# Optimization experiments

Hardware: AMD Instinct MI355X
Metric: run time of the kernel (lower is better)

The kernel has to match this reference:

```python
import jax, jax.numpy as jnp
import numpy as np

N = 100000
E = 1600000
IN_CH, HID_CH, OUT_CH = 128, 64, 32


def setup_inputs() -> dict:
    key = jax.random.key(0)
    ks = jax.random.split(key, 6)
    x = jax.random.normal(ks[0], (N, IN_CH), dtype=jnp.float32)
    ei = jax.random.randint(ks[1], (2, E), 0, N, dtype=jnp.int64)
    W1 = jax.random.normal(ks[2], (IN_CH, HID_CH), dtype=jnp.float32) * 0.05
    b1 = jax.random.normal(ks[3], (HID_CH,), dtype=jnp.float32) * 0.05
    W2 = jax.random.normal(ks[4], (HID_CH, OUT_CH), dtype=jnp.float32) * 0.05
    b2 = jax.random.normal(ks[5], (OUT_CH,), dtype=jnp.float32) * 0.05
    return {"x": x, "ei": ei, "W1": W1, "b1": b1, "W2": W2, "b2": b2}


def gcn_layer(x, sa, da, n):
    # degree with self-loops already appended in sa/da
    deg = jax.ops.segment_sum(jnp.ones((sa.shape[0],), x.dtype), da, num_segments=n)
    prod = deg[sa] * deg[da]
    norm = jnp.where(prod > 0, jax.lax.rsqrt(prod), 0.0)  # (deg_s*deg_d)^-0.5, inf->0
    msg = x[sa] * norm[:, None]            # [E+N, C] gather + scale
    return jax.ops.segment_sum(msg, da, num_segments=n)  # scatter_add


def reference(x, ei, W1, b1, W2, b2):
    n = x.shape[0]
    loop = jnp.arange(n, dtype=ei.dtype)
    sa = jnp.concatenate([ei[0], loop])
    da = jnp.concatenate([ei[1], loop])
    h = gcn_layer(x @ W1 + b1, sa, da, n)
    h = jax.nn.relu(h)
    # dropout: eval mode (training=False) -> identity
    return gcn_layer(h @ W2 + b2, sa, da, n)
```

## Files before the change

kernel.cpp:

```cpp
#include <hip/hip_runtime.h>

#define NN 100000
#define NE 1600000
#define IN_CH 128
#define HID_CH 64
#define OUT_CH 32
#define NBUCK 391
#define CHUNKA 8192

typedef unsigned short ushort_t;

__device__ inline ushort_t f2bf(float f) {
    union { float f; unsigned u; } v; v.f = f;
    unsigned r = v.u + 0x7fff + ((v.u >> 16) & 1);
    return (ushort_t)(r >> 16);
}
__device__ inline float blo(unsigned u) {
    union { unsigned x; float f; } v; v.x = u << 16; return v.f;
}
__device__ inline float bhi(unsigned u) {
    union { unsigned x; float f; } v; v.x = u & 0xffff0000u; return v.f;
}

__global__ __launch_bounds__(256) void k_bhist(const int* __restrict__ da,
                                               int* __restrict__ bcnt) {
    __shared__ int hist[NBUCK];
    int t = threadIdx.x;
    for (int i = t; i < NBUCK; i += 256) hist[i] = 0;
    __syncthreads();
    int base = blockIdx.x * CHUNKA;
    for (int i = 0; i < CHUNKA; i += 256) {
        int e = base + i + t;
        if (e < NE) atomicAdd(&hist[da[e] >> 8], 1);
    }
    __syncthreads();
    for (int i = t; i < NBUCK; i += 256) {
        int c = hist[i];
        if (c) atomicAdd(&bcnt[i], c);
    }
}

__global__ __launch_bounds__(512) void k_bscan(const int* __restrict__ bcnt,
                                               int* __restrict__ bbase,
                                               int* __restrict__ bcur,
                                               int* __restrict__ rowptr) {
    __shared__ int lds[512];
    int t = threadIdx.x;
    int v = (t < NBUCK) ? bcnt[t] : 0;
    lds[t] = v;
    __syncthreads();
    for (int off = 1; off < 512; off <<= 1) {
        int x = (t >= off) ? lds[t - off] : 0;
        __syncthreads();
        lds[t] += x;
        __syncthreads();
    }
    int excl = lds[t] - v;
    if (t < NBUCK) { bbase[t] = excl; bcur[t] = excl; }
    if (t == 0) { bbase[NBUCK] = NE; rowptr[NN] = NE; }
}

__global__ __launch_bounds__(256) void k_bfill(const int* __restrict__ sa,
                                               const int* __restrict__ da,
                                               int* __restrict__ bcur,
                                               unsigned* __restrict__ ebuf) {
    __shared__ int hist[NBUCK];
    __shared__ int lcur[NBUCK];
    int t = threadIdx.x;
    for (int i = t; i < NBUCK; i += 256) hist[i] = 0;
    __syncthreads();
    int base = blockIdx.x * CHUNKA;
    for (int i = 0; i < CHUNKA; i += 256) {
        int e = base + i + t;
        if (e < NE) atomicAdd(&hist[da[e] >> 8], 1);
    }
    __syncthreads();
    for (int b = t; b < NBUCK; b += 256) {
        int c = hist[b];
        lcur[b] = c ? atomicAdd(&bcur[b], c) : 0;
    }
    __syncthreads();
    for (int i = 0; i < CHUNKA; i += 256) {
        int e = base + i + t;
        if (e < NE) {
            int d = da[e];
            int p = atomicAdd(&lcur[d >> 8], 1);
            ebuf[p] = ((unsigned)sa[e] << 8) | (unsigned)(d & 255);
        }
    }
}

__global__ __launch_bounds__(256) void k_bfine(const unsigned* __restrict__ ebuf,
                                               const int* __restrict__ bbase,
                                               int* __restrict__ rowptr,
                                               float* __restrict__ rs,
                                               int* __restrict__ col) {
    __shared__ int cnt[256];
    __shared__ int cur[256];
    __shared__ int scn[256];
    int b = blockIdx.x, t = threadIdx.x;
    int nb = NN - b * 256; if (nb > 256) nb = 256;
    int beg = bbase[b], end = bbase[b + 1];
    cnt[t] = 0;
    __syncthreads();
    for (int i = beg + t; i < end; i += 256) atomicAdd(&cnt[ebuf[i] & 255], 1);
    __syncthreads();
    int v = cnt[t];
    scn[t] = v;
    __syncthreads();
    for (int off = 1; off < 256; off <<= 1) {
        int x = (t >= off) ? scn[t - off] : 0;
        __syncthreads();
        scn[t] += x;
        __syncthreads();
    }
    int excl = scn[t] - v;
    if (t < nb) {
        rowptr[b * 256 + t] = beg + excl;
        rs[b * 256 + t] = rsqrtf((float)(v + 1));
        cur[t] = beg + excl;
    }
    __syncthreads();
    for (int i = beg + t; i < end; i += 256) {
        unsigned p = ebuf[i];
        int pos = atomicAdd(&cur[p & 255], 1);
        col[pos] = (int)(p >> 8);
    }
}

#define SWZ1(n, k) ((n) * 128 + ((k) ^ ((((n) & 7)) << 2)))
#define SWZ2(n, k) ((n) * 64 + ((k) ^ ((((n) & 7)) << 2)))

__global__ __launch_bounds__(256) void k_gemm1(
    const float* __restrict__ x, const float* __restrict__ W1,
    const float* __restrict__ b1, const float* __restrict__ rs,
    ushort_t* __restrict__ xsb) {
    __shared__ float xt[64 * 128];
    __shared__ float w1s[128 * 64];
    int t = threadIdx.x;
    int base = blockIdx.x * 64;

#pragma unroll
    for (int i = 0; i < 8; ++i) {
        int flat = i * 1024 + t * 4;
        int node = flat >> 7, k0 = flat & 127;
        int gn = base + node;
        float4 v = make_float4(0.f, 0.f, 0.f, 0.f);
        if (gn < NN) v = *(const float4*)(x + (size_t)gn * IN_CH + k0);
        *(float4*)&xt[SWZ1(node, k0)] = v;
        *(float4*)&w1s[flat] = *(const float4*)(W1 + flat);
    }
    __syncthreads();

    int tn = t & 15, tc = t >> 4;
    int c0 = tc * 4;
    float acc[4][4];
#pragma unroll
    for (int a = 0; a < 4; ++a)
#pragma unroll
        for (int b = 0; b < 4; ++b) acc[a][b] = 0.f;

    for (int k0 = 0; k0 < 128; k0 += 4) {
        float xq[4][4], wq[4][4];
#pragma unroll
        for (int j = 0; j < 4; ++j)
            *(float4*)&wq[j][0] = *(float4*)&w1s[(k0 + j) * 64 + c0];
#pragma unroll
        for (int jn = 0; jn < 4; ++jn)
            *(float4*)&xq[jn][0] = *(float4*)&xt[SWZ1(tn + jn * 16, k0)];
#pragma unroll
        for (int jn = 0; jn < 4; ++jn)
#pragma unroll
            for (int j = 0; j < 4; ++j)
#pragma unroll
                for (int jc = 0; jc < 4; ++jc)
                    acc[jn][jc] = fmaf(xq[jn][j], wq[j][jc], acc[jn][jc]);
    }

    float4 bb = *(const float4*)&b1[c0];
#pragma unroll
    for (int jn = 0; jn < 4; ++jn) {
        int gn = base + tn + jn * 16;
        if (gn < NN) {
            float r = rs[gn];
            uint2 pk;
            pk.x = (unsigned)f2bf((acc[jn][0] + bb.x) * r) |
                   ((unsigned)f2bf((acc[jn][1] + bb.y) * r) << 16);
            pk.y = (unsigned)f2bf((acc[jn][2] + bb.z) * r) |
                   ((unsigned)f2bf((acc[jn][3] + bb.w) * r) << 16);
            *(uint2*)&xsb[(size_t)gn * HID_CH + c0] = pk;
        }
    }
}

__global__ __launch_bounds__(256) void k_agg1(
    const int* __restrict__ rowptr, const int* __restrict__ col,
    const ushort_t* __restrict__ xsb, const float* __restrict__ rs,
    float* __restrict__ h) {
    int gid = blockIdx.x * blockDim.x + threadIdx.x;
    int n = gid >> 6;
    if (n >= NN) return;
    int lane = threadIdx.x & 63;
    int g = lane >> 4;
    unsigned c0 = (unsigned)(lane & 15) * 4;
    int beg = rowptr[n], end = rowptr[n + 1];

    float a0 = 0.f, a1 = 0.f, a2 = 0.f, a3 = 0.f;
    if (g == 0) {
        uint2 sv = *(const uint2*)&xsb[(unsigned)n * 64u + c0];
        a0 = blo(sv.x); a1 = bhi(sv.x); a2 = blo(sv.y); a3 = bhi(sv.y);
    }

    int i = beg;
    for (; i + 8 <= end; i += 8) {
        int s0 = col[i + g];
        int s1 = col[i + 4 + g];
        uint2 v0 = *(const uint2*)&xsb[(unsigned)s0 * 64u + c0];
        uint2 v1 = *(const uint2*)&xsb[(unsigned)s1 * 64u + c0];
        a0 += blo(v0.x); a1 += bhi(v0.x); a2 += blo(v0.y); a3 += bhi(v0.y);
        a0 += blo(v1.x); a1 += bhi(v1.x); a2 += blo(v1.y); a3 += bhi(v1.y);
    }
    if (i + 4 <= end) {
        int s0 = col[i + g];
        uint2 v0 = *(const uint2*)&xsb[(unsigned)s0 * 64u + c0];
        a0 += blo(v0.x); a1 += bhi(v0.x); a2 += blo(v0.y); a3 += bhi(v0.y);
        i += 4;
    }
    int r = end - i;
    if (g < r) {
        int s0 = col[i + g];
        uint2 v0 = *(const uint2*)&xsb[(unsigned)s0 * 64u + c0];
        a0 += blo(v0.x); a1 += bhi(v0.x); a2 += blo(v0.y); a3 += bhi(v0.y);
    }

    a0 += __shfl_xor(a0, 16); a1 += __shfl_xor(a1, 16);
    a2 += __shfl_xor(a2, 16); a3 += __shfl_xor(a3, 16);
    a0 += __shfl_xor(a0, 32); a1 += __shfl_xor(a1, 32);
    a2 += __shfl_xor(a2, 32); a3 += __shfl_xor(a3, 32);

    if (g == 0) {
        float rn = rs[n];
        float4 o;
        o.x = fmaxf(a0 * rn, 0.f);
        o.y = fmaxf(a1 * rn, 0.f);
        o.z = fmaxf(a2 * rn, 0.f);
        o.w = fmaxf(a3 * rn, 0.f);
        *(float4*)&h[(size_t)n * HID_CH + c0] = o;
    }
}

__global__ __launch_bounds__(256) void k_gemm2(
    const float* __restrict__ h, const float* __restrict__ W2,
    const float* __restrict__ b2, const float* __restrict__ rs,
    ushort_t* __restrict__ ysb) {
    __shared__ float ht[64 * 64];
    __shared__ float w2s[64 * 32];
    int t = threadIdx.x;
    int base = blockIdx.x * 64;

#pragma unroll
    for (int i = 0; i < 4; ++i) {
        int flat = i * 1024 + t * 4;
        int node = flat >> 6, k0 = flat & 63;
        int gn = base + node;
        float4 v = make_float4(0.f, 0.f, 0.f, 0.f);
        if (gn < NN) v = *(const float4*)(h + (size_t)gn * HID_CH + k0);
        *(float4*)&ht[SWZ2(node, k0)] = v;
    }
#pragma unroll
    for (int i = 0; i < 2; ++i) {
        int flat = i * 1024 + t * 4;
        *(float4*)&w2s[flat] = *(const float4*)(W2 + flat);
    }
    __syncthreads();

    int tn = t & 15, tc = t >> 4;
    int c0 = tc * 2;
    float acc[4][2];
#pragma unroll
    for (int a = 0; a < 4; ++a) { acc[a][0] = 0.f; acc[a][1] = 0.f; }

    for (int k0 = 0; k0 < 64; k0 += 4) {
        float xq[4][4], wq[4][2];
#pragma unroll
        for (int j = 0; j < 4; ++j)
            *(float2*)&wq[j][0] = *(float2*)&w2s[(k0 + j) * 32 + c0];
#pragma unroll
        for (int jn = 0; jn < 4; ++jn)
            *(float4*)&xq[jn][0] = *(float4*)&ht[SWZ2(tn + jn * 16, k0)];
#pragma unroll
        for (int jn = 0; jn < 4; ++jn)
#pragma unroll
            for (int j = 0; j < 4; ++j) {
                acc[jn][0] = fmaf(xq[jn][j], wq[j][0], acc[jn][0]);
                acc[jn][1] = fmaf(xq[jn][j], wq[j][1], acc[jn][1]);
            }
    }

    float2 bb = *(const float2*)&b2[c0];
#pragma unroll
    for (int jn = 0; jn < 4; ++jn) {
        int gn = base + tn + jn * 16;
        if (gn < NN) {
            float r = rs[gn];
            unsigned pk = (unsigned)f2bf((acc[jn][0] + bb.x) * r) |
                          ((unsigned)f2bf((acc[jn][1] + bb.y) * r) << 16);
            *(unsigned*)&ysb[(size_t)gn * OUT_CH + c0] = pk;
        }
    }
}

__global__ __launch_bounds__(256) void k_agg2(
    const int* __restrict__ rowptr, const int* __restrict__ col,
    const ushort_t* __restrict__ ysb, const float* __restrict__ rs,
    float* __restrict__ out) {
    int gid = blockIdx.x * blockDim.x + threadIdx.x;
    int n = gid >> 6;
    if (n >= NN) return;
    int lane = threadIdx.x & 63;
    int g = lane >> 3;
    unsigned c0 = (unsigned)(lane & 7) * 4;
    int beg = rowptr[n], end = rowptr[n + 1];

    float a0 = 0.f, a1 = 0.f, a2 = 0.f, a3 = 0.f;
    if (g == 0) {
        uint2 sv = *(const uint2*)&ysb[(unsigned)n * 32u + c0];
        a0 = blo(sv.x); a1 = bhi(sv.x); a2 = blo(sv.y); a3 = bhi(sv.y);
    }

    int i = beg;
    for (; i + 16 <= end; i += 16) {
        int s0 = col[i + g];
        int s1 = col[i + 8 + g];
        uint2 v0 = *(const uint2*)&ysb[(unsigned)s0 * 32u + c0];
        uint2 v1 = *(const uint2*)&ysb[(unsigned)s1 * 32u + c0];
        a0 += blo(v0.x); a1 += bhi(v0.x); a2 += blo(v0.y); a3 += bhi(v0.y);
        a0 += blo(v1.x); a1 += bhi(v1.x); a2 += blo(v1.y); a3 += bhi(v1.y);
    }
    if (i + 8 <= end) {
        int s0 = col[i + g];
        uint2 v0 = *(const uint2*)&ysb[(unsigned)s0 * 32u + c0];
        a0 += blo(v0.x); a1 += bhi(v0.x); a2 += blo(v0.y); a3 += bhi(v0.y);
        i += 8;
    }
    int r = end - i;
    if (g < r) {
        int s0 = col[i + g];
        uint2 v0 = *(const uint2*)&ysb[(unsigned)s0 * 32u + c0];
        a0 += blo(v0.x); a1 += bhi(v0.x); a2 += blo(v0.y); a3 += bhi(v0.y);
    }

    a0 += __shfl_xor(a0, 8);  a1 += __shfl_xor(a1, 8);
    a2 += __shfl_xor(a2, 8);  a3 += __shfl_xor(a3, 8);
    a0 += __shfl_xor(a0, 16); a1 += __shfl_xor(a1, 16);
    a2 += __shfl_xor(a2, 16); a3 += __shfl_xor(a3, 16);
    a0 += __shfl_xor(a0, 32); a1 += __shfl_xor(a1, 32);
    a2 += __shfl_xor(a2, 32); a3 += __shfl_xor(a3, 32);

    if (g == 0) {
        float rn = rs[n];
        float4 o;
        o.x = a0 * rn; o.y = a1 * rn; o.z = a2 * rn; o.w = a3 * rn;
        *(float4*)&out[(size_t)n * OUT_CH + c0] = o;
    }
}

extern "C" void kernel_launch(void* const* d_in, const int* in_sizes, int n_in,
                              void* d_out, int out_size, void* d_ws, size_t ws_size,
                              hipStream_t stream) {
    const float* x  = (const float*)d_in[0];
    const int*   ei = (const int*)d_in[1];
    const float* W1 = (const float*)d_in[2];
    const float* b1 = (const float*)d_in[3];
    const float* W2 = (const float*)d_in[4];
    const float* b2 = (const float*)d_in[5];
    const int* sa = ei;
    const int* da = ei + NE;

    char* ws = (char*)d_ws;
    size_t off = 0;
    auto alloc = [&](size_t bytes) {
        void* p = ws + off;
        off += (bytes + 255) & ~(size_t)255;
        return p;
    };
    int*      bcnt   = (int*)alloc((size_t)NBUCK * 4);
    int*      bbase  = (int*)alloc((size_t)(NBUCK + 1) * 4);
    int*      bcur   = (int*)alloc((size_t)NBUCK * 4);
    int*      rowptr = (int*)alloc((size_t)(NN + 1) * 4);
    float*    rs     = (float*)alloc((size_t)NN * 4);
    unsigned* ebuf   = (unsigned*)alloc((size_t)NE * 4);
    int*      col    = (int*)alloc((size_t)NE * 4);
    ushort_t* xsb    = (ushort_t*)alloc((size_t)NN * HID_CH * 2);
    float*    hbuf   = (float*)alloc((size_t)NN * HID_CH * 4);
    ushort_t* ysb    = xsb;
    float*    outp   = (float*)d_out;

    const int B = 256;
    const int NBLKA = (NE + CHUNKA - 1) / CHUNKA;
    hipMemsetAsync(bcnt, 0, (size_t)NBUCK * 4, stream);
    k_bhist<<<NBLKA, 256, 0, stream>>>(da, bcnt);
    k_bscan<<<1, 512, 0, stream>>>(bcnt, bbase, bcur, rowptr);
    k_bfill<<<NBLKA, 256, 0, stream>>>(sa, da, bcur, ebuf);
    k_bfine<<<NBUCK, 256, 0, stream>>>(ebuf, bbase, rowptr, rs, col);

    const int NBLK_GEMM = (NN + 63) / 64;
    k_gemm1<<<NBLK_GEMM, 256, 0, stream>>>(x, W1, b1, rs, xsb);
    k_agg1<<<(NN * 64 + B - 1) / B, B, 0, stream>>>(rowptr, col, xsb, rs, hbuf);
    k_gemm2<<<NBLK_GEMM, 256, 0, stream>>>(hbuf, W2, b2, rs, ysb);
    k_agg2<<<(NN * 64 + B - 1) / B, B, 0, stream>>>(rowptr, col, ysb, rs, outp);
}
```

Measured before the change: 222.6 us.

## Fuse layer-1 aggregation with second GEMM and store x tile as bf16 in LDS

The first aggregation kernel now computes the relu'd hidden row in registers and immediately multiplies it by W2 with wave shuffles, writing bf16 y directly. This removes the fp32 hidden buffer round trip and the separate gemm2 launch. The aggregation loop is also unrolled to 16 edges. gemm1 packs its x tile into bf16 in shared memory to halve LDS use and allow more blocks per CU. That adds a bf16 rounding of the input x and puts per-node serial shuffle work into the aggregation.

Measured after the change: 221.0 us. Within noise of the previous version (-0.7%).

```diff
diff --git a/kernel.cpp b/kernel.cpp
--- a/kernel.cpp
+++ b/kernel.cpp
@@ -128,14 +128,13 @@
     }
 }
 
-#define SWZ1(n, k) ((n) * 128 + ((k) ^ ((((n) & 7)) << 2)))
-#define SWZ2(n, k) ((n) * 64 + ((k) ^ ((((n) & 7)) << 2)))
-
-__global__ __launch_bounds__(256) void k_gemm1(
+#define SWZU1(n, k2) ((n) * 64 + ((k2) ^ ((((n) & 7)) << 2)))
+
+__global__ __launch_bounds__(256, 3) void k_gemm1(
     const float* __restrict__ x, const float* __restrict__ W1,
     const float* __restrict__ b1, const float* __restrict__ rs,
     ushort_t* __restrict__ xsb) {
-    __shared__ float xt[64 * 128];
+    __shared__ unsigned xtb[64 * 64];
     __shared__ float w1s[128 * 64];
     int t = threadIdx.x;
     int base = blockIdx.x * 64;
@@ -147,7 +146,10 @@
         int gn = base + node;
         float4 v = make_float4(0.f, 0.f, 0.f, 0.f);
         if (gn < NN) v = *(const float4*)(x + (size_t)gn * IN_CH + k0);
-        *(float4*)&xt[SWZ1(node, k0)] = v;
+        uint2 pk;
+        pk.x = (unsigned)f2bf(v.x) | ((unsigned)f2bf(v.y) << 16);
+        pk.y = (unsigned)f2bf(v.z) | ((unsigned)f2bf(v.w) << 16);
+        *(uint2*)&xtb[SWZU1(node, k0 >> 1)] = pk;
         *(float4*)&w1s[flat] = *(const float4*)(W1 + flat);
     }
     __syncthreads();
@@ -161,13 +163,17 @@
         for (int b = 0; b < 4; ++b) acc[a][b] = 0.f;
 
     for (int k0 = 0; k0 < 128; k0 += 4) {
+        int k2 = k0 >> 1;
         float xq[4][4], wq[4][4];
 #pragma unroll
         for (int j = 0; j < 4; ++j)
             *(float4*)&wq[j][0] = *(float4*)&w1s[(k0 + j) * 64 + c0];
 #pragma unroll
-        for (int jn = 0; jn < 4; ++jn)
-            *(float4*)&xq[jn][0] = *(float4*)&xt[SWZ1(tn + jn * 16, k0)];
+        for (int jn = 0; jn < 4; ++jn) {
+            uint2 xu = *(uint2*)&xtb[SWZU1(tn + jn * 16, k2)];
+            xq[jn][0] = blo(xu.x); xq[jn][1] = bhi(xu.x);
+            xq[jn][2] = blo(xu.y); xq[jn][3] = bhi(xu.y);
+        }
 #pragma unroll
         for (int jn = 0; jn < 4; ++jn)
 #pragma unroll
@@ -193,14 +199,24 @@
     }
 }
 
-__global__ __launch_bounds__(256) void k_agg1(
+__global__ __launch_bounds__(512) void k_agg1g2(
     const int* __restrict__ rowptr, const int* __restrict__ col,
     const ushort_t* __restrict__ xsb, const float* __restrict__ rs,
-    float* __restrict__ h) {
-    int gid = blockIdx.x * blockDim.x + threadIdx.x;
-    int n = gid >> 6;
+    const float* __restrict__ W2, const float* __restrict__ b2,
+    ushort_t* __restrict__ ysb) {
+    __shared__ float w2s[HID_CH * OUT_CH];
+    __shared__ float b2s[OUT_CH];
+    int t = threadIdx.x;
+    {
+        int flat = t * 4;
+        *(float4*)&w2s[flat] = *(const float4*)(W2 + flat);
+        if (t < OUT_CH) b2s[t] = b2[t];
+    }
+    __syncthreads();
+
+    int n = blockIdx.x * 8 + (t >> 6);
     if (n >= NN) return;
-    int lane = threadIdx.x & 63;
+    int lane = t & 63;
     int g = lane >> 4;
     unsigned c0 = (unsigned)(lane & 15) * 4;
     int beg = rowptr[n], end = rowptr[n + 1];
@@ -212,19 +228,24 @@
     }
 
     int i = beg;
-    for (; i + 8 <= end; i += 8) {
+    for (; i + 16 <= end; i += 16) {
         int s0 = col[i + g];
         int s1 = col[i + 4 + g];
+        int s2 = col[i + 8 + g];
+        int s3 = col[i + 12 + g];
         uint2 v0 = *(const uint2*)&xsb[(unsigned)s0 * 64u + c0];
         uint2 v1 = *(const uint2*)&xsb[(unsigned)s1 * 64u + c0];
+        uint2 v2 = *(const uint2*)&xsb[(unsigned)s2 * 64u + c0];
+        uint2 v3 = *(const uint2*)&xsb[(unsigned)s3 * 64u + c0];
         a0 += blo(v0.x); a1 += bhi(v0.x); a2 += blo(v0.y); a3 += bhi(v0.y);
         a0 += blo(v1.x); a1 += bhi(v1.x); a2 += blo(v1.y); a3 += bhi(v1.y);
-    }
-    if (i + 4 <= end) {
+        a0 += blo(v2.x); a1 += bhi(v2.x); a2 += blo(v2.y); a3 += bhi(v2.y);
+        a0 += blo(v3.x); a1 += bhi(v3.x); a2 += blo(v3.y); a3 += bhi(v3.y);
+    }
+    for (; i + 4 <= end; i += 4) {
         int s0 = col[i + g];
         uint2 v0 = *(const uint2*)&xsb[(unsigned)s0 * 64u + c0];
         a0 += blo(v0.x); a1 += bhi(v0.x); a2 += blo(v0.y); a3 += bhi(v0.y);
-        i += 4;
     }
     int r = end - i;
     if (g < r) {
@@ -238,75 +259,34 @@
     a0 += __shfl_xor(a0, 32); a1 += __shfl_xor(a1, 32);
     a2 += __shfl_xor(a2, 32); a3 += __shfl_xor(a3, 32);
 
-    if (g == 0) {
-        float rn = rs[n];
-        float4 o;
-        o.x = fmaxf(a0 * rn, 0.f);
-        o.y = fmaxf(a1 * rn, 0.f);
-        o.z = fmaxf(a2 * rn, 0.f);
-        o.w = fmaxf(a3 * rn, 0.f);
-        *(float4*)&h[(size_t)n * HID_CH + c0] = o;
-    }
-}
-
-__global__ __launch_bounds__(256) void k_gemm2(
-    const float* __restrict__ h, const float* __restrict__ W2,
-    const float* __restrict__ b2, const float* __restrict__ rs,
-    ushort_t* __restrict__ ysb) {
-    __shared__ float ht[64 * 64];
-    __shared__ float w2s[64 * 32];
-    int t = threadIdx.x;
-    int base = blockIdx.x * 64;
-
-#pragma unroll
-    for (int i = 0; i < 4; ++i) {
-        int flat = i * 1024 + t * 4;
-        int node = flat >> 6, k0 = flat & 63;
-        int gn = base + node;
-        float4 v = make_float4(0.f, 0.f, 0.f, 0.f);
-        if (gn < NN) v = *(const float4*)(h + (size_t)gn * HID_CH + k0);
-        *(float4*)&ht[SWZ2(node, k0)] = v;
-    }
-#pragma unroll
-    for (int i = 0; i < 2; ++i) {
-        int flat = i * 1024 + t * 4;
-        *(float4*)&w2s[flat] = *(const float4*)(W2 + flat);
-    }
-    __syncthreads();
-
-    int tn = t & 15, tc = t >> 4;
-    int c0 = tc * 2;
-    float acc[4][2];
-#pragma unroll
-    for (int a = 0; a < 4; ++a) { acc[a][0] = 0.f; acc[a][1] = 0.f; }
-
-    for (int k0 = 0; k0 < 64; k0 += 4) {
-        float xq[4][4], wq[4][2];
-#pragma unroll
-        for (int j = 0; j < 4; ++j)
-            *(float2*)&wq[j][0] = *(float2*)&w2s[(k0 + j) * 32 + c0];
-#pragma unroll
-        for (int jn = 0; jn < 4; ++jn)
-            *(float4*)&xq[jn][0] = *(float4*)&ht[SWZ2(tn + jn * 16, k0)];
-#pragma unroll
-        for (int jn = 0; jn < 4; ++jn)
-#pragma unroll
-            for (int j = 0; j < 4; ++j) {
-                acc[jn][0] = fmaf(xq[jn][j], wq[j][0], acc[jn][0]);
-                acc[jn][1] = fmaf(xq[jn][j], wq[j][1], acc[jn][1]);
-            }
-    }
-
-    float2 bb = *(const float2*)&b2[c0];
-#pragma unroll
-    for (int jn = 0; jn < 4; ++jn) {
-        int gn = base + tn + jn * 16;
-        if (gn < NN) {
-            float r = rs[gn];
-            unsigned pk = (unsigned)f2bf((acc[jn][0] + bb.x) * r) |
-                          ((unsigned)f2bf((acc[jn][1] + bb.y) * r) << 16);
-            *(unsigned*)&ysb[(size_t)gn * OUT_CH + c0] = pk;
-        }
+    float rn = rs[n];
+    a0 = fmaxf(a0 * rn, 0.f);
+    a1 = fmaxf(a1 * rn, 0.f);
+    a2 = fmaxf(a2 * rn, 0.f);
+    a3 = fmaxf(a3 * rn, 0.f);
+
+    int half = lane >> 5;
+    int c = lane & 31;
+    float y = half ? 0.f : b2s[c];
+#pragma unroll
+    for (int kc = 0; kc < 8; ++kc) {
+        int kk = half * 8 + kc;
+        float h0 = __shfl(a0, kk);
+        float h1 = __shfl(a1, kk);
+        float h2 = __shfl(a2, kk);
+        float h3 = __shfl(a3, kk);
+        y = fmaf(h0, w2s[(4 * kk + 0) * OUT_CH + c], y);
+        y = fmaf(h1, w2s[(4 * kk + 1) * OUT_CH + c], y);
+        y = fmaf(h2, w2s[(4 * kk + 2) * OUT_CH + c], y);
+        y = fmaf(h3, w2s[(4 * kk + 3) * OUT_CH + c], y);
+    }
+    y += __shfl_xor(y, 32);
+    y *= rn;
+
+    float ynext = __shfl_down(y, 1);
+    if (half == 0 && (lane & 1) == 0) {
+        unsigned pk = (unsigned)f2bf(y) | ((unsigned)f2bf(ynext) << 16);
+        *(unsigned*)&ysb[(unsigned)n * 32u + (unsigned)c] = pk;
     }
 }
 
@@ -392,8 +372,7 @@
     unsigned* ebuf   = (unsigned*)alloc((size_t)NE * 4);
     int*      col    = (int*)alloc((size_t)NE * 4);
     ushort_t* xsb    = (ushort_t*)alloc((size_t)NN * HID_CH * 2);
-    float*    hbuf   = (float*)alloc((size_t)NN * HID_CH * 4);
-    ushort_t* ysb    = xsb;
+    ushort_t* ysb    = (ushort_t*)alloc((size_t)NN * OUT_CH * 2);
     float*    outp   = (float*)d_out;
 
     const int B = 256;
@@ -406,7 +385,6 @@
 
     const int NBLK_GEMM = (NN + 63) / 64;
     k_gemm1<<<NBLK_GEMM, 256, 0, stream>>>(x, W1, b1, rs, xsb);
-    k_agg1<<<(NN * 64 + B - 1) / B, B, 0, stream>>>(rowptr, col, xsb, rs, hbuf);
-    k_gemm2<<<NBLK_GEMM, 256, 0, stream>>>(hbuf, W2, b2, rs, ysb);
+    k_agg1g2<<<(NN + 7) / 8, 512, 0, stream>>>(rowptr, col, xsb, rs, W2, b2, ysb);
     k_agg2<<<(NN * 64 + B - 1) / B, B, 0, stream>>>(rowptr, col, ysb, rs, outp);
 }
```

## Use fp16 dot2 in first GEMM, store hidden activations as bf16, unroll aggregation

Applied to the files above, without the earlier changes.

The first GEMM now packs x and W1 into fp16 pairs in shared memory and accumulates with the packed dot2 instruction. This halves LDS footprint and raises occupancy via launch bounds. The hidden activations after aggregation are written as bf16 instead of fp32, which halves the write/read traffic between agg1 and gemm2. The agg1 neighbor loop is unrolled to 16 edges per iteration for more memory-level parallelism. The risk is extra precision loss from fp16 inputs (x is normal, fine) and bf16 hidden activations.

After: 222.4 us. About the same (-0.1%).

```diff
diff --git a/kernel.cpp b/kernel.cpp
--- a/kernel.cpp
+++ b/kernel.cpp
@@ -9,6 +9,7 @@
 #define CHUNKA 8192
 
 typedef unsigned short ushort_t;
+typedef _Float16 half2_t __attribute__((ext_vector_type(2)));
 
 __device__ inline ushort_t f2bf(float f) {
     union { float f; unsigned u; } v; v.f = f;
@@ -20,6 +21,22 @@
 }
 __device__ inline float bhi(unsigned u) {
     union { unsigned x; float f; } v; v.x = u & 0xffff0000u; return v.f;
+}
+__device__ inline unsigned pkh(float a, float b) {
+    union { half2_t h; unsigned u; } v;
+    v.h[0] = (_Float16)a; v.h[1] = (_Float16)b;
+    return v.u;
+}
+__device__ inline half2_t u2h(unsigned u) {
+    union { unsigned u; half2_t h; } v; v.u = u; return v.h;
+}
+__device__ inline float fdot2(unsigned a, unsigned b, float c) {
+#if __has_builtin(__builtin_amdgcn_fdot2)
+    return __builtin_amdgcn_fdot2(u2h(a), u2h(b), c, false);
+#else
+    half2_t ha = u2h(a), hb = u2h(b);
+    return c + (float)ha[0] * (float)hb[0] + (float)ha[1] * (float)hb[1];
+#endif
 }
 
 __global__ __launch_bounds__(256) void k_bhist(const int* __restrict__ da,
@@ -128,15 +145,15 @@
     }
 }
 
-#define SWZ1(n, k) ((n) * 128 + ((k) ^ ((((n) & 7)) << 2)))
+#define SWZU1(n, k2) ((n) * 64 + ((k2) ^ ((((n) & 7)) << 2)))
 #define SWZ2(n, k) ((n) * 64 + ((k) ^ ((((n) & 7)) << 2)))
 
-__global__ __launch_bounds__(256) void k_gemm1(
+__global__ __launch_bounds__(256, 4) void k_gemm1(
     const float* __restrict__ x, const float* __restrict__ W1,
     const float* __restrict__ b1, const float* __restrict__ rs,
     ushort_t* __restrict__ xsb) {
-    __shared__ float xt[64 * 128];
-    __shared__ float w1s[128 * 64];
+    __shared__ unsigned xth[64 * 64];
+    __shared__ unsigned w1h[64 * 64];
     int t = threadIdx.x;
     int base = blockIdx.x * 64;
 
@@ -147,8 +164,18 @@
         int gn = base + node;
         float4 v = make_float4(0.f, 0.f, 0.f, 0.f);
         if (gn < NN) v = *(const float4*)(x + (size_t)gn * IN_CH + k0);
-        *(float4*)&xt[SWZ1(node, k0)] = v;
-        *(float4*)&w1s[flat] = *(const float4*)(W1 + flat);
+        uint2 pk;
+        pk.x = pkh(v.x, v.y);
+        pk.y = pkh(v.z, v.w);
+        *(uint2*)&xth[SWZU1(node, k0 >> 1)] = pk;
+    }
+#pragma unroll
+    for (int i = 0; i < 16; ++i) {
+        int idx = i * 256 + t;
+        int k2 = idx >> 6, c = idx & 63;
+        float f0 = W1[(2 * k2) * 64 + c];
+        float f1 = W1[(2 * k2 + 1) * 64 + c];
+        w1h[idx] = pkh(f0, f1);
     }
     __syncthreads();
 
@@ -160,21 +187,22 @@
 #pragma unroll
         for (int b = 0; b < 4; ++b) acc[a][b] = 0.f;
 
-    for (int k0 = 0; k0 < 128; k0 += 4) {
-        float xq[4][4], wq[4][4];
-#pragma unroll
-        for (int j = 0; j < 4; ++j)
-            *(float4*)&wq[j][0] = *(float4*)&w1s[(k0 + j) * 64 + c0];
+    for (int k2 = 0; k2 < 64; k2 += 2) {
+        uint2 xu[4];
 #pragma unroll
         for (int jn = 0; jn < 4; ++jn)
-            *(float4*)&xq[jn][0] = *(float4*)&xt[SWZ1(tn + jn * 16, k0)];
+            xu[jn] = *(uint2*)&xth[SWZU1(tn + jn * 16, k2)];
+        uint4 w0 = *(uint4*)&w1h[(k2 + 0) * 64 + c0];
+        uint4 w1 = *(uint4*)&w1h[(k2 + 1) * 64 + c0];
+        unsigned wq0[4] = {w0.x, w0.y, w0.z, w0.w};
+        unsigned wq1[4] = {w1.x, w1.y, w1.z, w1.w};
 #pragma unroll
         for (int jn = 0; jn < 4; ++jn)
 #pragma unroll
-            for (int j = 0; j < 4; ++j)
-#pragma unroll
-                for (int jc = 0; jc < 4; ++jc)
-                    acc[jn][jc] = fmaf(xq[jn][j], wq[j][jc], acc[jn][jc]);
+            for (int jc = 0; jc < 4; ++jc) {
+                acc[jn][jc] = fdot2(xu[jn].x, wq0[jc], acc[jn][jc]);
+                acc[jn][jc] = fdot2(xu[jn].y, wq1[jc], acc[jn][jc]);
+            }
     }
 
     float4 bb = *(const float4*)&b1[c0];
@@ -196,7 +224,7 @@
 __global__ __launch_bounds__(256) void k_agg1(
     const int* __restrict__ rowptr, const int* __restrict__ col,
     const ushort_t* __restrict__ xsb, const float* __restrict__ rs,
-    float* __restrict__ h) {
+    ushort_t* __restrict__ hb) {
     int gid = blockIdx.x * blockDim.x + threadIdx.x;
     int n = gid >> 6;
     if (n >= NN) return;
@@ -212,19 +240,24 @@
     }
 
     int i = beg;
-    for (; i + 8 <= end; i += 8) {
+    for (; i + 16 <= end; i += 16) {
         int s0 = col[i + g];
         int s1 = col[i + 4 + g];
+        int s2 = col[i + 8 + g];
+        int s3 = col[i + 12 + g];
         uint2 v0 = *(const uint2*)&xsb[(unsigned)s0 * 64u + c0];
         uint2 v1 = *(const uint2*)&xsb[(unsigned)s1 * 64u + c0];
+        uint2 v2 = *(const uint2*)&xsb[(unsigned)s2 * 64u + c0];
+        uint2 v3 = *(const uint2*)&xsb[(unsigned)s3 * 64u + c0];
         a0 += blo(v0.x); a1 += bhi(v0.x); a2 += blo(v0.y); a3 += bhi(v0.y);
         a0 += blo(v1.x); a1 += bhi(v1.x); a2 += blo(v1.y); a3 += bhi(v1.y);
-    }
-    if (i + 4 <= end) {
+        a0 += blo(v2.x); a1 += bhi(v2.x); a2 += blo(v2.y); a3 += bhi(v2.y);
+        a0 += blo(v3.x); a1 += bhi(v3.x); a2 += blo(v3.y); a3 += bhi(v3.y);
+    }
+    for (; i + 4 <= end; i += 4) {
         int s0 = col[i + g];
         uint2 v0 = *(const uint2*)&xsb[(unsigned)s0 * 64u + c0];
         a0 += blo(v0.x); a1 += bhi(v0.x); a2 += blo(v0.y); a3 += bhi(v0.y);
-        i += 4;
     }
     int r = end - i;
     if (g < r) {
@@ -240,17 +273,17 @@
 
     if (g == 0) {
         float rn = rs[n];
-        float4 o;
-        o.x = fmaxf(a0 * rn, 0.f);
-        o.y = fmaxf(a1 * rn, 0.f);
-        o.z = fmaxf(a2 * rn, 0.f);
-        o.w = fmaxf(a3 * rn, 0.f);
-        *(float4*)&h[(size_t)n * HID_CH + c0] = o;
+        uint2 pk;
+        pk.x = (unsigned)f2bf(fmaxf(a0 * rn, 0.f)) |
+               ((unsigned)f2bf(fmaxf(a1 * rn, 0.f)) << 16);
+        pk.y = (unsigned)f2bf(fmaxf(a2 * rn, 0.f)) |
+               ((unsigned)f2bf(fmaxf(a3 * rn, 0.f)) << 16);
+        *(uint2*)&hb[(unsigned)n * 64u + c0] = pk;
     }
 }
 
 __global__ __launch_bounds__(256) void k_gemm2(
-    const float* __restrict__ h, const float* __restrict__ W2,
+    const ushort_t* __restrict__ hb, const float* __restrict__ W2,
     const float* __restrict__ b2, const float* __restrict__ rs,
     ushort_t* __restrict__ ysb) {
     __shared__ float ht[64 * 64];
@@ -259,13 +292,14 @@
     int base = blockIdx.x * 64;
 
 #pragma unroll
-    for (int i = 0; i < 4; ++i) {
-        int flat = i * 1024 + t * 4;
-        int node = flat >> 6, k0 = flat & 63;
+    for (int i = 0; i < 8; ++i) {
+        int uidx = i * 256 + t;
+        int node = uidx >> 5, k2 = uidx & 31;
         int gn = base + node;
-        float4 v = make_float4(0.f, 0.f, 0.f, 0.f);
-        if (gn < NN) v = *(const float4*)(h + (size_t)gn * HID_CH + k0);
-        *(float4*)&ht[SWZ2(node, k0)] = v;
+        unsigned u = 0;
+        if (gn < NN) u = *(const unsigned*)&hb[(size_t)gn * HID_CH + k2 * 2];
+        float2 f; f.x = blo(u); f.y = bhi(u);
+        *(float2*)&ht[SWZ2(node, k2 * 2)] = f;
     }
 #pragma unroll
     for (int i = 0; i < 2; ++i) {
@@ -392,8 +426,8 @@
     unsigned* ebuf   = (unsigned*)alloc((size_t)NE * 4);
     int*      col    = (int*)alloc((size_t)NE * 4);
     ushort_t* xsb    = (ushort_t*)alloc((size_t)NN * HID_CH * 2);
-    float*    hbuf   = (float*)alloc((size_t)NN * HID_CH * 4);
-    ushort_t* ysb    = xsb;
+    ushort_t* hb     = (ushort_t*)alloc((size_t)NN * HID_CH * 2);
+    ushort_t* ysb    = (ushort_t*)alloc((size_t)NN * OUT_CH * 2);
     float*    outp   = (float*)d_out;
 
     const int B = 256;
@@ -406,7 +440,7 @@
 
     const int NBLK_GEMM = (NN + 63) / 64;
     k_gemm1<<<NBLK_GEMM, 256, 0, stream>>>(x, W1, b1, rs, xsb);
-    k_agg1<<<(NN * 64 + B - 1) / B, B, 0, stream>>>(rowptr, col, xsb, rs, hbuf);
-    k_gemm2<<<NBLK_GEMM, 256, 0, stream>>>(hbuf, W2, b2, rs, ysb);
+    k_agg1<<<(NN * 64 + B - 1) / B, B, 0, stream>>>(rowptr, col, xsb, rs, hb);
+    k_gemm2<<<NBLK_GEMM, 256, 0, stream>>>(hb, W2, b2, rs, ysb);
     k_agg2<<<(NN * 64 + B - 1) / B, B, 0, stream>>>(rowptr, col, ysb, rs, outp);
 }
```
